# Performance work log

Hardware: AMD Instinct MI355X
Metric: run time of the kernel (lower is better)

## Reference

```python
import jax, jax.numpy as jnp
import numpy as np

DIM = 1024

def setup_inputs() -> dict:
    key = jax.random.key(0)
    ks = jax.random.split(key, 8)
    B, Sx, Sy, D = 4, 2048, 2048, DIM
    s = 1.0 / np.sqrt(D)
    return {
        "x": jax.random.normal(ks[0], (B, Sx, D), jnp.float32),
        "y": jax.random.normal(ks[1], (B, Sy, D), jnp.float32),
        "Wq": jax.random.normal(ks[2], (D, D), jnp.float32) * s,
        "bq": jnp.zeros((D,), jnp.float32),
        "Wk": jax.random.normal(ks[3], (D, D), jnp.float32) * s,
        "bk": jnp.zeros((D,), jnp.float32),
        "Wv": jax.random.normal(ks[4], (D, D), jnp.float32) * s,
        "bv": jnp.zeros((D,), jnp.float32),
    }

def reference(x, y, Wq, bq, Wk, bk, Wv, bv):
    D = x.shape[-1]
    scale = jnp.sqrt(jnp.asarray(D, x.dtype))
    Q = jnp.einsum('bsd,de->bse', x, Wq) + bq  # [B,Sx,D]
    K = jnp.einsum('btd,de->bte', y, Wk) + bk  # [B,Sy,D]
    V = jnp.einsum('btd,de->bte', y, Wv) + bv  # [B,Sy,D]
    scores = jnp.einsum('bse,bte->bst', Q, K) / scale  # [B,Sx,Sy]
    probs = jax.nn.softmax(scores, axis=-1)
    out = jnp.einsum('bst,bte->bse', probs, V)  # [B,Sx,D]
    return out
```

## Files before the change

### kernel.cpp

```cpp
#include <hip/hip_runtime.h>

typedef __bf16 bf16x8_t __attribute__((ext_vector_type(8)));
typedef float f32x16_t __attribute__((ext_vector_type(16)));
typedef unsigned short ushort_t;

__device__ __forceinline__ unsigned short f2bf(float f) {
  unsigned u = __float_as_uint(f);
  u = (u + 0x7FFFu + ((u >> 16) & 1u)) >> 16;
  return (unsigned short)u;
}
__device__ __forceinline__ float bf2f(unsigned short h) {
  return __uint_as_float(((unsigned)h) << 16);
}

__device__ __forceinline__ void gload16(const void* g, void* l) {
  __builtin_amdgcn_global_load_lds(
      (const __attribute__((address_space(1))) unsigned int*)g,
      (__attribute__((address_space(3))) unsigned int*)l, 16, 0, 0);
}

__global__ __launch_bounds__(256, 4)
void gemm_qkv(const float* __restrict__ X, const float* __restrict__ Y,
              const ushort_t* __restrict__ Bt, ushort_t* __restrict__ Cp,
              const float* __restrict__ bias)
{
  constexpr int ATILE = 4096;
  constexpr int BUFSZ = ATILE + 4096;
  __shared__ __align__(16) ushort_t sm[2 * BUFSZ];
  const int tid = threadIdx.x;
  const int lane = tid & 63;
  const int w = tid >> 6;
  const int wr = w >> 1, wc = w & 1;

  const int per = gridDim.x >> 3;
  int wg = blockIdx.x;
  wg = (wg & 7) * per + (wg >> 3);
  const int by = wg / 24, bx = wg - by * 24;
  const int bm = by * 128, bn = bx * 128;

  const float* Af = (bn >= 1024) ? Y : X;

  const int rA0 = (w * 2) * 16 + (lane >> 2);
  const int cA = ((lane & 3) ^ ((rA0 >> 1) & 3)) << 3;
  const float* pA0 = Af + (long)(bm + rA0) * 1024 + cA;
  const float* pA1 = pA0 + 16 * 1024;
  const ushort_t* pB0 = Bt + (long)(bn + rA0) * 1024 + cA;
  const ushort_t* pB1 = pB0 + 16 * 1024;

  auto stageB = [&](int kt, int buf) {
    const int k0 = kt << 5;
    ushort_t* s = sm + buf * BUFSZ;
    gload16(pB0 + k0, s + ATILE + (w * 2) * 512);
    gload16(pB1 + k0, s + ATILE + (w * 2 + 1) * 512);
  };

  float4 ra[2][2];
  auto loadA = [&](int kt) {
    const int k0 = kt << 5;
    ra[0][0] = *(const float4*)(pA0 + k0);
    ra[0][1] = *(const float4*)(pA0 + k0 + 4);
    ra[1][0] = *(const float4*)(pA1 + k0);
    ra[1][1] = *(const float4*)(pA1 + k0 + 4);
  };
  auto writeA = [&](int buf) {
    ushort_t* s = sm + buf * BUFSZ;
#pragma unroll
    for (int i = 0; i < 2; ++i) {
      uint4 o;
      o.x = (unsigned)f2bf(ra[i][0].x) | ((unsigned)f2bf(ra[i][0].y) << 16);
      o.y = (unsigned)f2bf(ra[i][0].z) | ((unsigned)f2bf(ra[i][0].w) << 16);
      o.z = (unsigned)f2bf(ra[i][1].x) | ((unsigned)f2bf(ra[i][1].y) << 16);
      o.w = (unsigned)f2bf(ra[i][1].z) | ((unsigned)f2bf(ra[i][1].w) << 16);
      *(uint4*)(s + (w * 2 + i) * 512 + lane * 8) = o;
    }
  };

  const int l31 = lane & 31, kh = lane >> 5;
  int offA[2][2], offB[2][2];
#pragma unroll
  for (int m = 0; m < 2; ++m) {
    const int row = wr * 64 + m * 32 + l31;
#pragma unroll
    for (int s = 0; s < 2; ++s)
      offA[m][s] = row * 32 + (((s * 2 + kh) ^ ((row >> 1) & 3)) << 3);
  }
#pragma unroll
  for (int n = 0; n < 2; ++n) {
    const int row = wc * 64 + n * 32 + l31;
#pragma unroll
    for (int s = 0; s < 2; ++s)
      offB[n][s] = ATILE + row * 32 + (((s * 2 + kh) ^ ((row >> 1) & 3)) << 3);
  }

  f32x16_t acc[2][2];
#pragma unroll
  for (int m = 0; m < 2; ++m)
#pragma unroll
    for (int n = 0; n < 2; ++n)
#pragma unroll
      for (int i = 0; i < 16; ++i) acc[m][n][i] = 0.f;

  loadA(0);
  stageB(0, 0);
  writeA(0);
  __syncthreads();

#define LDX(off) __builtin_bit_cast(bf16x8_t, *(const uint4*)(sp + (off)))
  const int nt = 1024 >> 5;
  for (int kt = 0; kt < nt; ++kt) {
    const int cur = kt & 1;
    const bool more = (kt + 1 < nt);
    if (more) { stageB(kt + 1, cur ^ 1); loadA(kt + 1); }
    const ushort_t* sp = sm + cur * BUFSZ;
    bf16x8_t af[2][2], bfv[2][2];
#pragma unroll
    for (int m = 0; m < 2; ++m)
#pragma unroll
      for (int s = 0; s < 2; ++s) af[m][s] = LDX(offA[m][s]);
#pragma unroll
    for (int n = 0; n < 2; ++n)
#pragma unroll
      for (int s = 0; s < 2; ++s) bfv[n][s] = LDX(offB[n][s]);
    __builtin_amdgcn_s_setprio(1);
#pragma unroll
    for (int s = 0; s < 2; ++s)
#pragma unroll
      for (int m = 0; m < 2; ++m)
#pragma unroll
        for (int n = 0; n < 2; ++n)
          acc[m][n] = __builtin_amdgcn_mfma_f32_32x32x16_bf16(
              af[m][s], bfv[n][s], acc[m][n], 0, 0, 0);
    __builtin_amdgcn_s_setprio(0);
    if (more) writeA(cur ^ 1);
    __syncthreads();
  }
#undef LDX

#pragma unroll
  for (int m = 0; m < 2; ++m) {
    const int growb = bm + wr * 64 + m * 32;
#pragma unroll
    for (int n = 0; n < 2; ++n) {
      const int gcol = bn + wc * 64 + n * 32 + l31;
      const float bv_ = bias[gcol];
#pragma unroll
      for (int r = 0; r < 16; ++r) {
        const int grow = growb + (r & 3) + 8 * (r >> 2) + 4 * kh;
        Cp[(long)grow * 3072 + gcol] = f2bf(acc[m][n][r] + bv_);
      }
    }
  }
}

template<int BN, int EPI>
__global__ __launch_bounds__((BN / 64) * 128, 2)
void gemm_big(const ushort_t* __restrict__ A, const ushort_t* __restrict__ Bt,
              void* __restrict__ Cp, float* __restrict__ aux,
              int gx, int gy, int K, int lda, int ldb, int ldc,
              long sA, long sB, long sC, float alpha)
{
  constexpr int WC = BN / 64;
  constexpr int NW = 2 * WC;
  constexpr int BUFSZ = 8192 + BN * 32;
  constexpr int A_SPW = 16 / NW;
  constexpr int B_SPW = (BN / 16) / NW;
  __shared__ __align__(16) ushort_t sm[2 * BUFSZ];

  const int tid = threadIdx.x;
  const int lane = tid & 63;
  const int w = tid >> 6;
  const int wr = w / WC, wc = w % WC;

  const int per = gridDim.x >> 3;
  int wg = blockIdx.x;
  wg = (wg & 7) * per + (wg >> 3);
  const int bz = wg / (gx * gy);
  const int rr = wg - bz * gx * gy;
  const int by = rr / gx, bx = rr - by * gx;
  const int bm = by * 256, bn = bx * BN;

  const int csw = (((lane & 3) ^ ((lane >> 3) & 3)) << 3);
  const ushort_t* pA = A + (long)bz * sA +
      (long)(bm + w * (A_SPW * 16) + (lane >> 2)) * lda + csw;
  const ushort_t* pB = Bt + (long)bz * sB +
      (long)(bn + w * (B_SPW * 16) + (lane >> 2)) * ldb + csw;

  auto stage = [&](int kt, int buf) {
    const int k0 = kt << 5;
    ushort_t* s = sm + buf * BUFSZ;
#pragma unroll
    for (int i = 0; i < A_SPW; ++i)
      gload16(pA + (long)(i * 16) * lda + k0, s + (w * A_SPW + i) * 512);
#pragma unroll
    for (int i = 0; i < B_SPW; ++i)
      gload16(pB + (long)(i * 16) * ldb + k0, s + 8192 + (w * B_SPW + i) * 512);
  };

  const int l31 = lane & 31, kh = lane >> 5;
  const int sw3 = (lane >> 1) & 3;
  int offA[4][2], offB[2][2];
#pragma unroll
  for (int mf = 0; mf < 4; ++mf)
#pragma unroll
    for (int ks = 0; ks < 2; ++ks)
      offA[mf][ks] = (wr * 128 + mf * 32 + l31) * 32 +
                     (((ks * 2 + kh) ^ sw3) << 3);
#pragma unroll
  for (int nf = 0; nf < 2; ++nf)
#pragma unroll
    for (int ks = 0; ks < 2; ++ks)
      offB[nf][ks] = 8192 + (wc * 64 + nf * 32 + l31) * 32 +
                     (((ks * 2 + kh) ^ sw3) << 3);

  f32x16_t acc[4][2];
#pragma unroll
  for (int m = 0; m < 4; ++m)
#pragma unroll
    for (int n = 0; n < 2; ++n)
#pragma unroll
      for (int i = 0; i < 16; ++i) acc[m][n][i] = 0.f;

  stage(0, 0);
  __syncthreads();

#define LDX(off) __builtin_bit_cast(bf16x8_t, *(const uint4*)(sp + (off)))
  const int nt = K >> 5;
  for (int kt = 0; kt < nt; ++kt) {
    const int cur = kt & 1;
    if (kt + 1 < nt) stage(kt + 1, cur ^ 1);
    const ushort_t* sp = sm + cur * BUFSZ;
    bf16x8_t af[4][2], bfv[2][2];
#pragma unroll
    for (int mf = 0; mf < 4; ++mf)
#pragma unroll
      for (int ks = 0; ks < 2; ++ks) af[mf][ks] = LDX(offA[mf][ks]);
#pragma unroll
    for (int nf = 0; nf < 2; ++nf)
#pragma unroll
      for (int ks = 0; ks < 2; ++ks) bfv[nf][ks] = LDX(offB[nf][ks]);
    __builtin_amdgcn_s_setprio(1);
#pragma unroll
    for (int ks = 0; ks < 2; ++ks)
#pragma unroll
      for (int mf = 0; mf < 4; ++mf)
#pragma unroll
        for (int nf = 0; nf < 2; ++nf)
          acc[mf][nf] = __builtin_amdgcn_mfma_f32_32x32x16_bf16(
              af[mf][ks], bfv[nf][ks], acc[mf][nf], 0, 0, 0);
    __builtin_amdgcn_s_setprio(0);
    __syncthreads();
  }
#undef LDX

  const long zC = (long)bz * sC;
  float* pf = (float*)sm;
  if constexpr (EPI == 1) {
    if (tid < 256) pf[tid] = 0.f;
    __syncthreads();
  }
#pragma unroll
  for (int mf = 0; mf < 4; ++mf) {
    const int growb = bm + wr * 128 + mf * 32;
    float part[16];
    if constexpr (EPI == 1) {
#pragma unroll
      for (int r = 0; r < 16; ++r) part[r] = 0.f;
    }
#pragma unroll
    for (int nf = 0; nf < 2; ++nf) {
      const int gcol = bn + wc * 64 + nf * 32 + l31;
#pragma unroll
      for (int r = 0; r < 16; ++r) {
        const int grow = growb + (r & 3) + 8 * (r >> 2) + 4 * kh;
        float v = acc[mf][nf][r] * alpha;
        if constexpr (EPI == 1) {
          const ushort_t pb = f2bf(__expf(v));
          ((ushort_t*)Cp)[zC + (long)grow * ldc + gcol] = pb;
          part[r] += bf2f(pb);
        } else if constexpr (EPI == 2) {
          v *= aux[bz * 2048 + grow];
          ((float*)Cp)[zC + (long)grow * ldc + gcol] = v;
        } else {
          ((ushort_t*)Cp)[zC + (long)grow * ldc + gcol] = f2bf(v);
        }
      }
    }
    if constexpr (EPI == 1) {
#pragma unroll
      for (int step = 1; step < 32; step <<= 1)
#pragma unroll
        for (int r = 0; r < 16; ++r) part[r] += __shfl_xor(part[r], step, 64);
      if (l31 == 0) {
#pragma unroll
        for (int r = 0; r < 16; ++r) {
          const int rloc = wr * 128 + mf * 32 + (r & 3) + 8 * (r >> 2) + 4 * kh;
          atomicAdd(&pf[rloc], part[r]);
        }
      }
    }
  }
  if constexpr (EPI == 1) {
    __syncthreads();
    if (tid < 256)
      aux[(long)bx * 8192 + bz * 2048 + by * 256 + tid] = pf[tid];
  }
}

__global__ __launch_bounds__(256)
void invrow(const float* __restrict__ psumG, float* __restrict__ inv) {
  const int r = blockIdx.x * 256 + threadIdx.x;
  float s = 0.f;
#pragma unroll
  for (int k = 0; k < 8; ++k) s += psumG[(long)k * 8192 + r];
  inv[r] = 1.0f / s;
}

__global__ __launch_bounds__(256)
void wtrans3(const float* __restrict__ W0, const float* __restrict__ W1,
             const float* __restrict__ W2, ushort_t* __restrict__ T0,
             ushort_t* __restrict__ T1, ushort_t* __restrict__ T2) {
  const float* W = (blockIdx.z == 0) ? W0 : (blockIdx.z == 1) ? W1 : W2;
  ushort_t* Wt = (blockIdx.z == 0) ? T0 : (blockIdx.z == 1) ? T1 : T2;
  __shared__ float tile[32][33];
  const int bx = blockIdx.x * 32;
  const int by = blockIdx.y * 32;
  const int t = threadIdx.x;
  const int c = t & 31, r0 = t >> 5;
#pragma unroll
  for (int i = 0; i < 4; ++i)
    tile[r0 + i * 8][c] = W[(long)(by + r0 + i * 8) * 1024 + bx + c];
  __syncthreads();
#pragma unroll
  for (int i = 0; i < 4; ++i)
    Wt[(long)(bx + r0 + i * 8) * 1024 + by + c] = f2bf(tile[c][r0 + i * 8]);
}

__global__ __launch_bounds__(256)
void bconcat3(const float* __restrict__ a, const float* __restrict__ b,
              const float* __restrict__ c, float* __restrict__ o) {
  const int i = blockIdx.x * 256 + threadIdx.x;
  o[i] = (i < 1024) ? a[i] : (i < 2048) ? b[i - 1024] : c[i - 2048];
}

__global__ __launch_bounds__(256)
void transpose_bf16(const ushort_t* __restrict__ in, ushort_t* __restrict__ out,
                    int ld_in, int ld_out, long in_bs, long out_bs) {
  __shared__ ushort_t tt[64][65];
  in += (long)blockIdx.z * in_bs;
  out += (long)blockIdx.z * out_bs;
  const int r0 = blockIdx.y * 64, c0 = blockIdx.x * 64;
  const int tc = threadIdx.x & 31;
  const int tr = threadIdx.x >> 5;
#pragma unroll
  for (int i = 0; i < 8; ++i) {
    const unsigned v = *(const unsigned*)(in + (long)(r0 + tr + 8 * i) * ld_in + c0 + tc * 2);
    tt[tr + 8 * i][tc * 2] = (ushort_t)(v & 0xffff);
    tt[tr + 8 * i][tc * 2 + 1] = (ushort_t)(v >> 16);
  }
  __syncthreads();
#pragma unroll
  for (int i = 0; i < 8; ++i) {
    const unsigned v = (unsigned)tt[tc * 2][tr + 8 * i] |
                       ((unsigned)tt[tc * 2 + 1][tr + 8 * i] << 16);
    *(unsigned*)(out + (long)(c0 + tr + 8 * i) * ld_out + r0 + tc * 2) = v;
  }
}

extern "C" void kernel_launch(void* const* d_in, const int* in_sizes, int n_in,
                              void* d_out, int out_size, void* d_ws, size_t ws_size,
                              hipStream_t stream) {
  const float* x  = (const float*)d_in[0];
  const float* y  = (const float*)d_in[1];
  const float* Wq = (const float*)d_in[2];
  const float* bq = (const float*)d_in[3];
  const float* Wk = (const float*)d_in[4];
  const float* bk = (const float*)d_in[5];
  const float* Wv = (const float*)d_in[6];
  const float* bv = (const float*)d_in[7];
  float* out = (float*)d_out;

  const int D = 1024;
  const long MB_ = 1l << 20;

  ushort_t* ws   = (ushort_t*)d_ws;
  ushort_t* Wall = ws;
  ushort_t* QKV8 = ws + 3 * MB_;
  ushort_t* Sb   = ws + 27 * MB_;
  ushort_t* Vt   = ws + 43 * MB_;
  float*    bias3 = (float*)(ws + 51 * MB_);
  float*    psumG = (float*)(ws + 51 * MB_ + 8192);
  float*    inv   = psumG + 8 * 8192;

  dim3 blk(256);

  wtrans3<<<dim3(32, 32, 3), blk, 0, stream>>>(
      Wq, Wk, Wv, Wall, Wall + 1 * MB_, Wall + 2 * MB_);
  bconcat3<<<dim3(12), blk, 0, stream>>>(bq, bk, bv, bias3);

  gemm_qkv<<<dim3(1536), blk, 0, stream>>>(x, y, Wall, QKV8, bias3);

  transpose_bf16<<<dim3(16, 32, 4), blk, 0, stream>>>(
      QKV8 + 2048, Vt, 3072, 2048, 2048l * 3072, 1024l * 2048);

  gemm_big<256, 1><<<dim3(256), dim3(512), 0, stream>>>(
      QKV8, QKV8 + 1024, Sb, psumG,
      8, 8, D, 3072, 3072, 2048,
      2048l * 3072, 2048l * 3072, 2048l * 2048, 0.03125f);

  invrow<<<dim3(32), blk, 0, stream>>>(psumG, inv);

  gemm_big<128, 2><<<dim3(256), blk, 0, stream>>>(
      Sb, Vt, out, inv,
      8, 8, 2048, 2048, 2048, D,
      2048l * 2048, 1024l * 2048, 2048l * 1024, 1.0f);
}
```

Baseline: 202.8 us.

## Pre-convert inputs to bf16, DMA both GEMM operands, write V transposed directly

A single prep kernel now converts x and y to bf16 and also performs the weight transpose and bias concatenation, replacing three launches with one. The QKV GEMM then loads both A and B tiles straight into LDS with global_load_lds instead of loading fp32 A into registers and converting it in the loop. Its epilogue writes the V columns directly in transposed layout, which removes the separate transpose kernel. In exchange the bf16 copies of x and y take an extra round trip through memory, and the transposed V stores are strided 8-byte writes.

```diff
diff --git a/kernel.cpp b/kernel.cpp
--- a/kernel.cpp
+++ b/kernel.cpp
@@ -20,12 +20,12 @@
 }
 
 __global__ __launch_bounds__(256, 4)
-void gemm_qkv(const float* __restrict__ X, const float* __restrict__ Y,
-              const ushort_t* __restrict__ Bt, ushort_t* __restrict__ Cp,
-              const float* __restrict__ bias)
+void gemm_qkv2(const ushort_t* __restrict__ Xb, const ushort_t* __restrict__ Yb,
+               const ushort_t* __restrict__ Bt, ushort_t* __restrict__ Cp,
+               ushort_t* __restrict__ Vt, const float* __restrict__ bias)
 {
   constexpr int ATILE = 4096;
-  constexpr int BUFSZ = ATILE + 4096;
+  constexpr int BUFSZ = 8192;
   __shared__ __align__(16) ushort_t sm[2 * BUFSZ];
   const int tid = threadIdx.x;
   const int lane = tid & 63;
@@ -38,43 +38,24 @@
   const int by = wg / 24, bx = wg - by * 24;
   const int bm = by * 128, bn = bx * 128;
 
-  const float* Af = (bn >= 1024) ? Y : X;
-
-  const int rA0 = (w * 2) * 16 + (lane >> 2);
-  const int cA = ((lane & 3) ^ ((rA0 >> 1) & 3)) << 3;
-  const float* pA0 = Af + (long)(bm + rA0) * 1024 + cA;
-  const float* pA1 = pA0 + 16 * 1024;
-  const ushort_t* pB0 = Bt + (long)(bn + rA0) * 1024 + cA;
+  const ushort_t* Ab = (bn >= 1024) ? Yb : Xb;
+
+  const int r0 = (w * 2) * 16 + (lane >> 2);
+  const int csw = (((lane & 3) ^ ((r0 >> 1) & 3)) << 3);
+  const ushort_t* pA0 = Ab + (long)(bm + r0) * 1024 + csw;
+  const ushort_t* pA1 = pA0 + 16 * 1024;
+  const ushort_t* pB0 = Bt + (long)(bn + r0) * 1024 + csw;
   const ushort_t* pB1 = pB0 + 16 * 1024;
 
-  auto stageB = [&](int kt, int buf) {
+  auto stage = [&](int kt, int buf) {
     const int k0 = kt << 5;
     ushort_t* s = sm + buf * BUFSZ;
+    gload16(pA0 + k0, s + (w * 2) * 512);
+    gload16(pA1 + k0, s + (w * 2 + 1) * 512);
     gload16(pB0 + k0, s + ATILE + (w * 2) * 512);
     gload16(pB1 + k0, s + ATILE + (w * 2 + 1) * 512);
   };
 
-  float4 ra[2][2];
-  auto loadA = [&](int kt) {
-    const int k0 = kt << 5;
-    ra[0][0] = *(const float4*)(pA0 + k0);
-    ra[0][1] = *(const float4*)(pA0 + k0 + 4);
-    ra[1][0] = *(const float4*)(pA1 + k0);
-    ra[1][1] = *(const float4*)(pA1 + k0 + 4);
-  };
-  auto writeA = [&](int buf) {
-    ushort_t* s = sm + buf * BUFSZ;
-#pragma unroll
-    for (int i = 0; i < 2; ++i) {
-      uint4 o;
-      o.x = (unsigned)f2bf(ra[i][0].x) | ((unsigned)f2bf(ra[i][0].y) << 16);
-      o.y = (unsigned)f2bf(ra[i][0].z) | ((unsigned)f2bf(ra[i][0].w) << 16);
-      o.z = (unsigned)f2bf(ra[i][1].x) | ((unsigned)f2bf(ra[i][1].y) << 16);
-      o.w = (unsigned)f2bf(ra[i][1].z) | ((unsigned)f2bf(ra[i][1].w) << 16);
-      *(uint4*)(s + (w * 2 + i) * 512 + lane * 8) = o;
-    }
-  };
-
   const int l31 = lane & 31, kh = lane >> 5;
   int offA[2][2], offB[2][2];
 #pragma unroll
@@ -100,17 +81,14 @@
 #pragma unroll
       for (int i = 0; i < 16; ++i) acc[m][n][i] = 0.f;
 
-  loadA(0);
-  stageB(0, 0);
-  writeA(0);
+  stage(0, 0);
   __syncthreads();
 
 #define LDX(off) __builtin_bit_cast(bf16x8_t, *(const uint4*)(sp + (off)))
-  const int nt = 1024 >> 5;
+  const int nt = 32;
   for (int kt = 0; kt < nt; ++kt) {
     const int cur = kt & 1;
-    const bool more = (kt + 1 < nt);
-    if (more) { stageB(kt + 1, cur ^ 1); loadA(kt + 1); }
+    if (kt + 1 < nt) stage(kt + 1, cur ^ 1);
     const ushort_t* sp = sm + cur * BUFSZ;
     bf16x8_t af[2][2], bfv[2][2];
 #pragma unroll
@@ -131,7 +109,6 @@
           acc[m][n] = __builtin_amdgcn_mfma_f32_32x32x16_bf16(
               af[m][s], bfv[n][s], acc[m][n], 0, 0, 0);
     __builtin_amdgcn_s_setprio(0);
-    if (more) writeA(cur ^ 1);
     __syncthreads();
   }
 #undef LDX
@@ -143,10 +120,26 @@
     for (int n = 0; n < 2; ++n) {
       const int gcol = bn + wc * 64 + n * 32 + l31;
       const float bv_ = bias[gcol];
-#pragma unroll
-      for (int r = 0; r < 16; ++r) {
-        const int grow = growb + (r & 3) + 8 * (r >> 2) + 4 * kh;
-        Cp[(long)grow * 3072 + gcol] = f2bf(acc[m][n][r] + bv_);
+      if (gcol < 2048) {
+#pragma unroll
+        for (int r = 0; r < 16; ++r) {
+          const int grow = growb + (r & 3) + 8 * (r >> 2) + 4 * kh;
+          Cp[(long)grow * 3072 + gcol] = f2bf(acc[m][n][r] + bv_);
+        }
+      } else {
+        const int d = gcol - 2048;
+#pragma unroll
+        for (int rq = 0; rq < 4; ++rq) {
+          const int t0 = growb + 8 * rq + 4 * kh;
+          const int b = t0 >> 11, tt = t0 & 2047;
+          unsigned long long w4 =
+                (unsigned long long)f2bf(acc[m][n][rq * 4 + 0] + bv_)
+              | ((unsigned long long)f2bf(acc[m][n][rq * 4 + 1] + bv_) << 16)
+              | ((unsigned long long)f2bf(acc[m][n][rq * 4 + 2] + bv_) << 32)
+              | ((unsigned long long)f2bf(acc[m][n][rq * 4 + 3] + bv_) << 48);
+          *(unsigned long long*)(Vt + (long)b * (1024l * 2048) +
+                                 (long)d * 2048 + tt) = w4;
+        }
       }
     }
   }
@@ -316,53 +309,49 @@
 }
 
 __global__ __launch_bounds__(256)
-void wtrans3(const float* __restrict__ W0, const float* __restrict__ W1,
-             const float* __restrict__ W2, ushort_t* __restrict__ T0,
-             ushort_t* __restrict__ T1, ushort_t* __restrict__ T2) {
-  const float* W = (blockIdx.z == 0) ? W0 : (blockIdx.z == 1) ? W1 : W2;
-  ushort_t* Wt = (blockIdx.z == 0) ? T0 : (blockIdx.z == 1) ? T1 : T2;
-  __shared__ float tile[32][33];
-  const int bx = blockIdx.x * 32;
-  const int by = blockIdx.y * 32;
+void prep(const float* __restrict__ x, const float* __restrict__ y,
+          const float* __restrict__ W0, const float* __restrict__ W1,
+          const float* __restrict__ W2,
+          const float* __restrict__ b0, const float* __restrict__ b1,
+          const float* __restrict__ b2,
+          ushort_t* __restrict__ xb, ushort_t* __restrict__ yb,
+          ushort_t* __restrict__ Wall, float* __restrict__ bias3)
+{
+  const int gid = blockIdx.x;
   const int t = threadIdx.x;
-  const int c = t & 31, r0 = t >> 5;
-#pragma unroll
-  for (int i = 0; i < 4; ++i)
-    tile[r0 + i * 8][c] = W[(long)(by + r0 + i * 8) * 1024 + bx + c];
-  __syncthreads();
-#pragma unroll
-  for (int i = 0; i < 4; ++i)
-    Wt[(long)(bx + r0 + i * 8) * 1024 + by + c] = f2bf(tile[c][r0 + i * 8]);
-}
-
-__global__ __launch_bounds__(256)
-void bconcat3(const float* __restrict__ a, const float* __restrict__ b,
-              const float* __restrict__ c, float* __restrict__ o) {
-  const int i = blockIdx.x * 256 + threadIdx.x;
-  o[i] = (i < 1024) ? a[i] : (i < 2048) ? b[i - 1024] : c[i - 2048];
-}
-
-__global__ __launch_bounds__(256)
-void transpose_bf16(const ushort_t* __restrict__ in, ushort_t* __restrict__ out,
-                    int ld_in, int ld_out, long in_bs, long out_bs) {
-  __shared__ ushort_t tt[64][65];
-  in += (long)blockIdx.z * in_bs;
-  out += (long)blockIdx.z * out_bs;
-  const int r0 = blockIdx.y * 64, c0 = blockIdx.x * 64;
-  const int tc = threadIdx.x & 31;
-  const int tr = threadIdx.x >> 5;
-#pragma unroll
-  for (int i = 0; i < 8; ++i) {
-    const unsigned v = *(const unsigned*)(in + (long)(r0 + tr + 8 * i) * ld_in + c0 + tc * 2);
-    tt[tr + 8 * i][tc * 2] = (ushort_t)(v & 0xffff);
-    tt[tr + 8 * i][tc * 2 + 1] = (ushort_t)(v >> 16);
-  }
-  __syncthreads();
-#pragma unroll
-  for (int i = 0; i < 8; ++i) {
-    const unsigned v = (unsigned)tt[tc * 2][tr + 8 * i] |
-                       ((unsigned)tt[tc * 2 + 1][tr + 8 * i] << 16);
-    *(unsigned*)(out + (long)(c0 + tr + 8 * i) * ld_out + r0 + tc * 2) = v;
+  if (gid < 8192) {
+    const float* in = (gid < 4096) ? x : y;
+    ushort_t* outp = (gid < 4096) ? xb : yb;
+    const long i = (long)(gid & 4095) * 256 + t;
+    const float4 a = ((const float4*)in)[i * 2];
+    const float4 c = ((const float4*)in)[i * 2 + 1];
+    uint4 o;
+    o.x = (unsigned)f2bf(a.x) | ((unsigned)f2bf(a.y) << 16);
+    o.y = (unsigned)f2bf(a.z) | ((unsigned)f2bf(a.w) << 16);
+    o.z = (unsigned)f2bf(c.x) | ((unsigned)f2bf(c.y) << 16);
+    o.w = (unsigned)f2bf(c.z) | ((unsigned)f2bf(c.w) << 16);
+    ((uint4*)outp)[i] = o;
+  } else if (gid < 11264) {
+    const int wgi = gid - 8192;
+    const int z = wgi >> 10;
+    const int rsub = wgi & 1023;
+    const int bx = (rsub & 31) * 32;
+    const int by = (rsub >> 5) * 32;
+    const float* W = (z == 0) ? W0 : (z == 1) ? W1 : W2;
+    ushort_t* Wt = Wall + (long)z * (1024l * 1024);
+    __shared__ float tile[32][33];
+    const int c = t & 31, r0 = t >> 5;
+#pragma unroll
+    for (int i = 0; i < 4; ++i)
+      tile[r0 + i * 8][c] = W[(long)(by + r0 + i * 8) * 1024 + bx + c];
+    __syncthreads();
+#pragma unroll
+    for (int i = 0; i < 4; ++i)
+      Wt[(long)(bx + r0 + i * 8) * 1024 + by + c] = f2bf(tile[c][r0 + i * 8]);
+  } else {
+    const int i = (gid - 11264) * 256 + t;
+    if (i < 3072)
+      bias3[i] = (i < 1024) ? b0[i] : (i < 2048) ? b1[i - 1024] : b2[i - 2048];
   }
 }
 
@@ -386,6 +375,8 @@
   ushort_t* Wall = ws;
   ushort_t* QKV8 = ws + 3 * MB_;
   ushort_t* Sb   = ws + 27 * MB_;
+  ushort_t* yb   = ws + 27 * MB_;
+  ushort_t* xb   = ws + 35 * MB_;
   ushort_t* Vt   = ws + 43 * MB_;
   float*    bias3 = (float*)(ws + 51 * MB_);
   float*    psumG = (float*)(ws + 51 * MB_ + 8192);
@@ -393,14 +384,10 @@
 
   dim3 blk(256);
 
-  wtrans3<<<dim3(32, 32, 3), blk, 0, stream>>>(
-      Wq, Wk, Wv, Wall, Wall + 1 * MB_, Wall + 2 * MB_);
-  bconcat3<<<dim3(12), blk, 0, stream>>>(bq, bk, bv, bias3);
-
-  gemm_qkv<<<dim3(1536), blk, 0, stream>>>(x, y, Wall, QKV8, bias3);
-
-  transpose_bf16<<<dim3(16, 32, 4), blk, 0, stream>>>(
-      QKV8 + 2048, Vt, 3072, 2048, 2048l * 3072, 1024l * 2048);
+  prep<<<dim3(11276), blk, 0, stream>>>(
+      x, y, Wq, Wk, Wv, bq, bk, bv, xb, yb, Wall, bias3);
+
+  gemm_qkv2<<<dim3(1536), blk, 0, stream>>>(xb, yb, Wall, QKV8, Vt, bias3);
 
   gemm_big<256, 1><<<dim3(256), dim3(512), 0, stream>>>(
       QKV8, QKV8 + 1024, Sb, psumG,
```

New measurement: 192.3 us. -5.2%, faster.
